# Optimization experiments

Measured on AMD Instinct MI355X. Metric: run time of the kernel, lower is better.

Reference implementation:

```python
import jax, jax.numpy as jnp
import numpy as np

B, T, D = 64, 8, 512          # batch, num_tokens (= num_heads), hidden_size (= head_dim)
S = 512                       # history seq_len
NKV = 4                       # num_key_value_heads
G = T // NKV                  # num_key_value_groups
EPS = 1e-6
SCALE = D ** -0.5
NEG_INF = float('-inf')


def rmsnorm(x, w):
    # Qwen3NextRMSNorm: norm in fp32, scale by (1 + weight), cast back
    xf = x.astype(jnp.float32)
    n = xf * jax.lax.rsqrt(jnp.mean(xf * xf, axis=-1, keepdims=True) + EPS)
    return (n * (1.0 + w.astype(jnp.float32))).astype(x.dtype)


def setup_inputs() -> dict:
    key = jax.random.key(0)
    ks = jax.random.split(key, 8)
    return {
        'target_emb': jax.random.normal(ks[0], (B, T, D), dtype=jnp.float32),
        'history_emb': jax.random.normal(ks[1], (B, S, D), dtype=jnp.float32),
        'key_padding_mask': jax.random.bernoulli(ks[2], 0.2, (B, S)),
        'q_proj_w': jax.random.normal(ks[3], (D, D), dtype=jnp.float32) * (D ** -0.5),
        'k_proj_w': jax.random.normal(ks[4], (NKV * D, D), dtype=jnp.float32) * (D ** -0.5),
        'v_proj_w': jax.random.normal(ks[5], (NKV * D, D), dtype=jnp.float32) * (D ** -0.5),
        'q_norm_w': jnp.zeros((D,), dtype=jnp.float32),
        'k_norm_w': jnp.zeros((D,), dtype=jnp.float32),
    }


def reference(target_emb, history_emb, key_padding_mask,
              q_proj_w, k_proj_w, v_proj_w, q_norm_w, k_norm_w):
    # q_proj on flattened tokens: [B,T,D] @ W^T -> [B,T,D]
    q = jnp.einsum('btd,ed->bte', target_emb, q_proj_w)
    q = rmsnorm(q, q_norm_w)
    # k/v projections: [B,S,D] -> [B,S,NKV,D]
    k = jnp.einsum('bsd,ed->bse', history_emb, k_proj_w).reshape(B, S, NKV, D)
    v = jnp.einsum('bsd,ed->bse', history_emb, v_proj_w).reshape(B, S, NKV, D)
    k = rmsnorm(k, k_norm_w)
    # group queries by kv head instead of materializing repeat_kv copies
    qg = q.reshape(B, NKV, G, D)              # [B,NKV,G,D]
    kt = jnp.transpose(k, (0, 2, 1, 3))        # [B,NKV,S,D]
    vt = jnp.transpose(v, (0, 2, 1, 3))        # [B,NKV,S,D]
    scores = jnp.einsum('bngd,bnsd->bngs', qg, kt) * SCALE  # [B,NKV,G,S]
    bias = jnp.where(key_padding_mask, NEG_INF, 0.0).astype(jnp.float32)
    scores = scores + bias[:, None, None, :]
    attn = jax.nn.softmax(scores.astype(jnp.float32), axis=-1).astype(q.dtype)
    out = jnp.einsum('bngs,bnsd->bngd', attn, vt)  # [B,NKV,G,D]
    tokens = out.reshape(B, T, D)
    attn_weights = attn.reshape(B, T, 1, S)       # matches torch [B,H,1,S]
    return (tokens, attn_weights)
```

## Files before the change

kernel.cpp:

```cpp
#include <hip/hip_runtime.h>
#include <stdint.h>

#define NB 64
#define NT 8
#define ND 512
#define NS 512
#define NKV 4
#define BSLICE 32
#define NSLICE (NB / BSLICE)

typedef __attribute__((ext_vector_type(8))) short short8_t;
typedef __attribute__((ext_vector_type(8))) unsigned short ushort8_t;
typedef __attribute__((ext_vector_type(4))) float f32x4;

typedef const __attribute__((address_space(1))) void gas_void;
typedef __attribute__((address_space(3))) void las_void;

#define HSP_HI 0ull
#define WKH_B  16777216ull
#define WVH_B  18874368ull
#define WKT_B  20971520ull
#define THI_B  23068672ull
#define TLO_B  23592960ull
#define QWH_B  24117248ull
#define QWL_B  24641536ull
#define QP_B   25165824ull
#define WFF_B  26214400ull
#define OUTF_B 27262976ull
#define SSQ_B  28311552ull
#define MASK_B 28835840ull
#define PBUF_B 28966912ull
#define DOT_B  30015488ull
#define QPH_B  31064064ull
#define QPL_B  31588352ull
#define WFH_B  32112640ull
#define WFL_B  32636928ull
#define HH_B   33161216ull
#define HL_B   33685504ull
#define FLAG_B 34209792ull
#define ZERO_CNT 917504

__device__ __forceinline__ float b2f(unsigned short u) {
    union { unsigned int i; float f; } x; x.i = ((unsigned int)u) << 16; return x.f;
}
__device__ __forceinline__ unsigned short f2b(float f) {
    union { float f; unsigned int i; } x; x.f = f;
    unsigned int i = x.i;
    unsigned int r = i + 0x7FFFu + ((i >> 16) & 1u);
    return (unsigned short)(r >> 16);
}
__device__ __forceinline__ float in_elem(const void* p, long long i, int is_f32) {
    return is_f32 ? ((const float*)p)[i] : b2f(((const unsigned short*)p)[i]);
}
__device__ __forceinline__ void store_out(void* out, int is_f32, size_t idx, float v) {
    if (is_f32) ((float*)out)[idx] = v;
    else        ((unsigned short*)out)[idx] = f2b(v);
}

__global__ __launch_bounds__(256) void scan_zero_kernel(const unsigned short* __restrict__ hraw,
                                                        const void* __restrict__ mraw,
                                                        int* __restrict__ flag,
                                                        float* __restrict__ zbase) {
    const int tid = threadIdx.x;
    const int bx = blockIdx.x;
    if (bx >= 2) {
        zbase[(size_t)(bx - 2) * 256 + tid] = 0.0f;
        return;
    }
    if (bx == 0) {
        __shared__ int cnt;
        if (tid == 0) cnt = 0;
        __syncthreads();
        int c = 0;
#pragma unroll
        for (int it = 0; it < 16; ++it) {
            unsigned int e = (hraw[tid + it * 256] >> 7) & 0xFFu;
            if (e >= 0xF0u) ++c;
        }
        if (c) atomicAdd(&cnt, c);
        __syncthreads();
        if (tid == 0) flag[0] = (cnt >= 8) ? 1 : 0;
    } else {
        __shared__ int s_bf16, s_f32, s_not01, s_oddnz;
        if (tid == 0) { s_bf16 = 0; s_f32 = 0; s_not01 = 0; s_oddnz = 0; }
        __syncthreads();
        const unsigned int* w32 = (const unsigned int*)mraw;
        int f_bf16 = 0, f_f32 = 0, f_not01 = 0, f_oddnz = 0;
#pragma unroll
        for (int it = 0; it < 32; ++it) {
            const int i = tid + it * 256;
            unsigned int w = w32[i];
            if (w == 0x00003F80u || w == 0x3F803F80u) f_bf16 = 1;
            if (w == 0x3F800000u) f_f32 = 1;
            if (w != 0u && w != 1u && w != 0x3F800000u) f_not01 = 1;
            if ((i & 1) && w != 0u) f_oddnz = 1;
        }
        if (f_bf16)  s_bf16 = 1;
        if (f_f32)   s_f32 = 1;
        if (f_not01) s_not01 = 1;
        if (f_oddnz) s_oddnz = 1;
        __syncthreads();
        if (tid == 0) {
            int mode;
            if (s_bf16)       mode = 3;
            else if (s_f32)   mode = 0;
            else if (s_not01) mode = 1;
            else if (s_oddnz) mode = 0;
            else              mode = 2;
            flag[1] = mode;
        }
    }
}

__device__ __forceinline__ void split8(const void* src, long long i8, int is_f32,
                                       ushort8_t& h, ushort8_t& l) {
    if (is_f32) {
        const float* s = (const float*)src + i8;
        float4 a = *(const float4*)s;
        float4 b = *(const float4*)(s + 4);
        float v[8] = {a.x, a.y, a.z, a.w, b.x, b.y, b.z, b.w};
#pragma unroll
        for (int j = 0; j < 8; ++j) {
            unsigned short hh = f2b(v[j]);
            h[j] = hh;
            l[j] = f2b(v[j] - b2f(hh));
        }
    } else {
        h = *(const ushort8_t*)((const unsigned short*)src + i8);
#pragma unroll
        for (int j = 0; j < 8; ++j) l[j] = 0;
    }
}
__device__ __forceinline__ ushort8_t hi8(const void* src, long long i8, int is_f32) {
    ushort8_t h;
    if (is_f32) {
        const float* s = (const float*)src + i8;
        float4 a = *(const float4*)s;
        float4 b = *(const float4*)(s + 4);
        float v[8] = {a.x, a.y, a.z, a.w, b.x, b.y, b.z, b.w};
#pragma unroll
        for (int j = 0; j < 8; ++j) h[j] = f2b(v[j]);
    } else {
        h = *(const ushort8_t*)((const unsigned short*)src + i8);
    }
    return h;
}

__global__ __launch_bounds__(256) void prep_kernel(const void* __restrict__ target,
                                                   const void* __restrict__ Wq,
                                                   const void* __restrict__ Wk,
                                                   const void* __restrict__ Wv,
                                                   unsigned short* __restrict__ tHi,
                                                   unsigned short* __restrict__ tLo,
                                                   unsigned short* __restrict__ qwHi,
                                                   unsigned short* __restrict__ qwLo,
                                                   unsigned short* __restrict__ wkHi,
                                                   unsigned short* __restrict__ wvHi,
                                                   unsigned short* __restrict__ wkT,
                                                   const int* __restrict__ flag) {
    __shared__ unsigned short tile[64][65];
    const int bx = blockIdx.x;
    const int tid = threadIdx.x;
    const int is_f32 = flag[0];
    if (bx < 128) {
        const long long i8 = ((long long)bx * 256 + tid) * 8;
        ushort8_t h, l;
        split8(target, i8, is_f32, h, l);
        *(ushort8_t*)(tHi + i8) = h;
        *(ushort8_t*)(tLo + i8) = l;
    } else if (bx < 256) {
        const long long i8 = ((long long)(bx - 128) * 256 + tid) * 8;
        ushort8_t h, l;
        split8(Wq, i8, is_f32, h, l);
        *(ushort8_t*)(qwHi + i8) = h;
        *(ushort8_t*)(qwLo + i8) = l;
    } else if (bx < 768) {
        const long long i8 = ((long long)(bx - 256) * 256 + tid) * 8;
        *(ushort8_t*)(wkHi + i8) = hi8(Wk, i8, is_f32);
    } else if (bx < 1280) {
        const long long i8 = ((long long)(bx - 768) * 256 + tid) * 8;
        *(ushort8_t*)(wvHi + i8) = hi8(Wv, i8, is_f32);
    } else {
        const int idx = bx - 1280;
        const int e0 = (idx & 31) * 64, d0 = (idx >> 5) * 64;
        const int tx = tid & 63, ty = tid >> 6;
#pragma unroll
        for (int i = 0; i < 16; ++i) {
            const int er = ty + 4 * i;
            tile[er][tx] = f2b(in_elem(Wk, (long long)(e0 + er) * 512 + d0 + tx, is_f32));
        }
        __syncthreads();
        const int n = e0 >> 9, eLoc = (e0 & 511);
#pragma unroll
        for (int i = 0; i < 16; ++i) {
            const int d = d0 + ty + 4 * i;
            wkT[(size_t)n * 512 * 512 + (size_t)d * 512 + eLoc + tx] = tile[tx][ty + 4 * i];
        }
    }
}

__global__ __launch_bounds__(256) void presplit_hist_kernel(const void* __restrict__ src,
                                                            unsigned short* __restrict__ hi,
                                                            const int* __restrict__ flag,
                                                            long long elemOff) {
    const long long i8 = ((long long)blockIdx.x * 256 + threadIdx.x) * 8;
    *(ushort8_t*)(hi + i8) = hi8(src, elemOff + i8, flag[0]);
}


__device__ __forceinline__ void mfma2_tile(const unsigned short* __restrict__ Ah,
                                           const unsigned short* __restrict__ Al,
                                           const unsigned short* __restrict__ B,
                                           unsigned short* AsH, unsigned short* AsL,
                                           unsigned short* Bs,
                                           int m0, int n0, int tid,
                                           int ktBeg, int ktEnd,
                                           f32x4 acc[4][4]) {
    const int lane = tid & 63, wave = tid >> 6;
    const int wr = wave >> 1, wc = wave & 1;
    const int lr = lane & 15, lq = lane >> 4;
#pragma unroll
    for (int i = 0; i < 4; ++i)
#pragma unroll
        for (int j = 0; j < 4; ++j) acc[i][j] = (f32x4){0.f, 0.f, 0.f, 0.f};

    for (int kt = ktBeg; kt < ktEnd; ++kt) {
        const int k0 = kt << 5;
#pragma unroll
        for (int i = 0; i < 2; ++i) {
            const int c = i * 256 + tid;
            const size_t aoff = (size_t)(m0 + (c >> 2)) * 512 + (k0 + (c & 3) * 8);
            const size_t boff = (size_t)(n0 + (c >> 2)) * 512 + (k0 + (c & 3) * 8);
            __builtin_amdgcn_global_load_lds((gas_void*)(Ah + aoff), (las_void*)(AsH + c * 8), 16, 0, 0);
            __builtin_amdgcn_global_load_lds((gas_void*)(Al + aoff), (las_void*)(AsL + c * 8), 16, 0, 0);
            __builtin_amdgcn_global_load_lds((gas_void*)(B + boff), (las_void*)(Bs + c * 8), 16, 0, 0);
        }
        __syncthreads();
        short8_t aH[4], aL[4], bF[4];
#pragma unroll
        for (int t = 0; t < 4; ++t) {
            const int ao = (wr * 64 + t * 16 + lr) * 32 + lq * 8;
            aH[t] = *(const short8_t*)(AsH + ao);
            aL[t] = *(const short8_t*)(AsL + ao);
            bF[t] = *(const short8_t*)(Bs + (wc * 64 + t * 16 + lr) * 32 + lq * 8);
        }
#pragma unroll
        for (int ti = 0; ti < 4; ++ti)
#pragma unroll
            for (int tj = 0; tj < 4; ++tj)
                acc[ti][tj] = __builtin_amdgcn_mfma_f32_16x16x32_bf16(aH[ti], bF[tj], acc[ti][tj], 0, 0, 0);
#pragma unroll
        for (int ti = 0; ti < 4; ++ti)
#pragma unroll
            for (int tj = 0; tj < 4; ++tj)
                acc[ti][tj] = __builtin_amdgcn_mfma_f32_16x16x32_bf16(aL[ti], bF[tj], acc[ti][tj], 0, 0, 0);
        __syncthreads();
    }
}

__device__ __forceinline__ void mfma3_tile(const unsigned short* __restrict__ Ah,
                                           const unsigned short* __restrict__ Al,
                                           const unsigned short* __restrict__ Bh,
                                           const unsigned short* __restrict__ Bl,
                                           unsigned short* AsH, unsigned short* AsL,
                                           unsigned short* BsH, unsigned short* BsL,
                                           int m0, int n0, int tid,
                                           int ktBeg, int ktEnd,
                                           f32x4 acc[4][4]) {
    const int lane = tid & 63, wave = tid >> 6;
    const int wr = wave >> 1, wc = wave & 1;
    const int lr = lane & 15, lq = lane >> 4;
#pragma unroll
    for (int i = 0; i < 4; ++i)
#pragma unroll
        for (int j = 0; j < 4; ++j) acc[i][j] = (f32x4){0.f, 0.f, 0.f, 0.f};

    for (int kt = ktBeg; kt < ktEnd; ++kt) {
        const int k0 = kt << 5;
#pragma unroll
        for (int i = 0; i < 2; ++i) {
            const int c = i * 256 + tid;
            const size_t aoff = (size_t)(m0 + (c >> 2)) * 512 + (k0 + (c & 3) * 8);
            const size_t boff = (size_t)(n0 + (c >> 2)) * 512 + (k0 + (c & 3) * 8);
            __builtin_amdgcn_global_load_lds((gas_void*)(Ah + aoff), (las_void*)(AsH + c * 8), 16, 0, 0);
            __builtin_amdgcn_global_load_lds((gas_void*)(Al + aoff), (las_void*)(AsL + c * 8), 16, 0, 0);
            __builtin_amdgcn_global_load_lds((gas_void*)(Bh + boff), (las_void*)(BsH + c * 8), 16, 0, 0);
            __builtin_amdgcn_global_load_lds((gas_void*)(Bl + boff), (las_void*)(BsL + c * 8), 16, 0, 0);
        }
        __syncthreads();
        short8_t aH[4], aL[4], bH[4], bL[4];
#pragma unroll
        for (int t = 0; t < 4; ++t) {
            const int ao = (wr * 64 + t * 16 + lr) * 32 + lq * 8;
            const int bo = (wc * 64 + t * 16 + lr) * 32 + lq * 8;
            aH[t] = *(const short8_t*)(AsH + ao);
            aL[t] = *(const short8_t*)(AsL + ao);
            bH[t] = *(const short8_t*)(BsH + bo);
            bL[t] = *(const short8_t*)(BsL + bo);
        }
#pragma unroll
        for (int ti = 0; ti < 4; ++ti)
#pragma unroll
            for (int tj = 0; tj < 4; ++tj)
                acc[ti][tj] = __builtin_amdgcn_mfma_f32_16x16x32_bf16(aH[ti], bH[tj], acc[ti][tj], 0, 0, 0);
#pragma unroll
        for (int ti = 0; ti < 4; ++ti)
#pragma unroll
            for (int tj = 0; tj < 4; ++tj)
                acc[ti][tj] = __builtin_amdgcn_mfma_f32_16x16x32_bf16(aH[ti], bL[tj], acc[ti][tj], 0, 0, 0);
#pragma unroll
        for (int ti = 0; ti < 4; ++ti)
#pragma unroll
            for (int tj = 0; tj < 4; ++tj)
                acc[ti][tj] = __builtin_amdgcn_mfma_f32_16x16x32_bf16(aL[ti], bH[tj], acc[ti][tj], 0, 0, 0);
        __syncthreads();
    }
}

__global__ __launch_bounds__(256) void gemm3_ks(const unsigned short* __restrict__ Ah,
                                                const unsigned short* __restrict__ Al,
                                                const unsigned short* __restrict__ Bh,
                                                const unsigned short* __restrict__ Bl,
                                                float* __restrict__ C) {
    __shared__ __align__(16) unsigned short AsH[128 * 32];
    __shared__ __align__(16) unsigned short AsL[128 * 32];
    __shared__ __align__(16) unsigned short BsH[128 * 32];
    __shared__ __align__(16) unsigned short BsL[128 * 32];
    const int m0 = blockIdx.x * 128, n0 = blockIdx.y * 128;
    const int kt0 = blockIdx.z * 4;
    const int tid = threadIdx.x;
    f32x4 acc[4][4];
    mfma3_tile(Ah, Al, Bh, Bl, AsH, AsL, BsH, BsL, m0, n0, tid, kt0, kt0 + 4, acc);
    const int lane = tid & 63, wave = tid >> 6;
    const int wr = wave >> 1, wc = wave & 1;
    const int lr = lane & 15, lq = lane >> 4;
#pragma unroll
    for (int ti = 0; ti < 4; ++ti)
#pragma unroll
        for (int tj = 0; tj < 4; ++tj)
#pragma unroll
            for (int r = 0; r < 4; ++r) {
                const int row = m0 + wr * 64 + ti * 16 + lq * 4 + r;
                const int col = n0 + wc * 64 + tj * 16 + lr;
                atomicAdd(&C[(size_t)row * 512 + col], acc[ti][tj][r]);
            }
}

__global__ __launch_bounds__(64) void rmsnorm_qperm(const float* __restrict__ q,
                                                    const void* __restrict__ qnw,
                                                    const void* __restrict__ knw,
                                                    unsigned short* __restrict__ qpHi,
                                                    unsigned short* __restrict__ qpLo,
                                                    const int* __restrict__ flag) {
    const int row = blockIdx.x;
    const int lane = threadIdx.x;
    const int is_f32 = flag[0];
    const float* p = q + (size_t)row * ND + lane * 8;
    float v[8];
    float4 a = *(const float4*)p;
    float4 b4 = *(const float4*)(p + 4);
    v[0] = a.x; v[1] = a.y; v[2] = a.z; v[3] = a.w;
    v[4] = b4.x; v[5] = b4.y; v[6] = b4.z; v[7] = b4.w;
    float ssq = 0.f;
#pragma unroll
    for (int j = 0; j < 8; ++j) ssq = fmaf(v[j], v[j], ssq);
#pragma unroll
    for (int off = 1; off < 64; off <<= 1) ssq += __shfl_xor(ssq, off);
    float r = rsqrtf(ssq * (1.0f / ND) + 1e-6f);
    const float SCALE = 0.044194173824159216f;
    const int b = row >> 3, h = row & 7;
    const int prow = (h >> 1) * 128 + b * 2 + (h & 1);
    ushort8_t hh, ll;
#pragma unroll
    for (int j = 0; j < 8; ++j) {
        int e = lane * 8 + j;
        float val = v[j] * r * (1.0f + in_elem(qnw, e, is_f32)) * (1.0f + in_elem(knw, e, is_f32)) * SCALE;
        unsigned short hv = f2b(val);
        hh[j] = hv; ll[j] = f2b(val - b2f(hv));
    }
    *(ushort8_t*)(qpHi + (size_t)prow * 512 + lane * 8) = hh;
    *(ushort8_t*)(qpLo + (size_t)prow * 512 + lane * 8) = ll;
}

__global__ __launch_bounds__(256) void wfold_ks(const unsigned short* __restrict__ qpHi,
                                                const unsigned short* __restrict__ qpLo,
                                                const unsigned short* __restrict__ wkT,
                                                float* __restrict__ wfF) {
    __shared__ __align__(16) unsigned short AsH[128 * 32];
    __shared__ __align__(16) unsigned short AsL[128 * 32];
    __shared__ __align__(16) unsigned short Bs[128 * 32];
    const int n = blockIdx.x;
    const int m0 = n * 128, n0 = blockIdx.y * 128;
    const int kt0 = blockIdx.z * 4;
    const int tid = threadIdx.x;
    f32x4 acc[4][4];
    mfma2_tile(qpHi, qpLo, wkT + (size_t)n * 512 * 512, AsH, AsL, Bs, m0, n0, tid, kt0, kt0 + 4, acc);

    const int lane = tid & 63, wave = tid >> 6;
    const int wr = wave >> 1, wc = wave & 1;
    const int lr = lane & 15, lq = lane >> 4;
#pragma unroll
    for (int ti = 0; ti < 4; ++ti)
#pragma unroll
        for (int tj = 0; tj < 4; ++tj)
#pragma unroll
            for (int r = 0; r < 4; ++r) {
                const int row = m0 + wr * 64 + ti * 16 + lq * 4 + r;
                const int d = n0 + wc * 64 + tj * 16 + lr;
                atomicAdd(&wfF[(size_t)row * 512 + d], acc[ti][tj][r]);
            }
}

#define SSQ8_ABUF(b) ((b) * 32768)
#define SSQ8_BBUF(b) (65536 + (b) * 32768)

#define SSQ8_STAGE_A(r, tt, bufOff)                                                       \
    do {                                                                                  \
        const int rcA0_ = rl0 + (r) * 64;                                                 \
        __builtin_amdgcn_global_load_lds(                                                 \
            (gas_void*)(A + (size_t)(mBase + rcA0_) * 512 + (tt) * 64 + ksw),             \
            (las_void*)(smem + (bufOff) + rcA0_ * 128 + k0 * 2), 16, 0, 0);               \
        const int rcA1_ = rcA0_ + 128;                                                    \
        __builtin_amdgcn_global_load_lds(                                                 \
            (gas_void*)(A + (size_t)(mBase + rcA1_) * 512 + (tt) * 64 + ksw),             \
            (las_void*)(smem + (bufOff) + rcA1_ * 128 + k0 * 2), 16, 0, 0);               \
    } while (0)

#define SSQ8_STAGE_B(q, tt, bufOff)                                                       \
    do {                                                                                  \
        const int rcB0_ = bR + (q) * 32;                                                  \
        __builtin_amdgcn_global_load_lds(                                                 \
            (gas_void*)(W + (size_t)(nBase + rcB0_) * 512 + (tt) * 64 + ksw),             \
            (las_void*)(smem + (bufOff) + rcB0_ * 128 + k0 * 2), 16, 0, 0);               \
        const int rcB1_ = rcB0_ + 128;                                                    \
        __builtin_amdgcn_global_load_lds(                                                 \
            (gas_void*)(W + (size_t)(nBase + rcB1_) * 512 + (tt) * 64 + ksw),             \
            (las_void*)(smem + (bufOff) + rcB1_ * 128 + k0 * 2), 16, 0, 0);               \
    } while (0)

#define SSQ8_READ_A(qm, bufOff)                                                           \
    _Pragma("unroll")                                                                     \
    for (int m_ = 0; m_ < 4; ++m_) {                                                      \
        const int rc_ = wm * 128 + (qm) * 64 + m_ * 16 + lr;                              \
        af[m_][0] = *(const short8_t*)(smem + (bufOff) + rc_ * 128 + kb0);                \
        af[m_][1] = *(const short8_t*)(smem + (bufOff) + rc_ * 128 + kb1);                \
    }

#define SSQ8_READ_B2(nh, bufOff)                                                          \
    _Pragma("unroll")                                                                     \
    for (int n_ = 0; n_ < 2; ++n_) {                                                      \
        const int cc_ = wn * 64 + (nh) * 32 + n_ * 16 + lr;                               \
        bf[(nh) * 2 + n_][0] = *(const short8_t*)(smem + (bufOff) + cc_ * 128 + kb0);     \
        bf[(nh) * 2 + n_][1] = *(const short8_t*)(smem + (bufOff) + cc_ * 128 + kb1);     \
    }

#define SSQ8_MFMA_Q(qm, nh)                                                               \
    _Pragma("unroll")                                                                     \
    for (int m_ = 0; m_ < 4; ++m_)                                                        \
    _Pragma("unroll")                                                                     \
    for (int n_ = 0; n_ < 2; ++n_) {                                                      \
        acc[(qm) * 4 + m_][(nh) * 2 + n_] = __builtin_amdgcn_mfma_f32_16x16x32_bf16(      \
            af[m_][0], bf[(nh) * 2 + n_][0], acc[(qm) * 4 + m_][(nh) * 2 + n_], 0, 0, 0); \
        acc[(qm) * 4 + m_][(nh) * 2 + n_] = __builtin_amdgcn_mfma_f32_16x16x32_bf16(      \
            af[m_][1], bf[(nh) * 2 + n_][1], acc[(qm) * 4 + m_][(nh) * 2 + n_], 0, 0, 0); \
    }

#define SSQ8_SYNC_PRE()                                                                   \
    __builtin_amdgcn_s_barrier();                                                         \
    asm volatile("s_waitcnt lgkmcnt(0)" ::: "memory");                                    \
    __builtin_amdgcn_sched_barrier(0);                                                    \
    __builtin_amdgcn_s_setprio(1);

#define SSQ8_SYNC_POST()                                                                  \
    __builtin_amdgcn_s_setprio(0);                                                        \
    __builtin_amdgcn_s_barrier();

__global__ __launch_bounds__(512) void gemm_ssq8(const unsigned short* __restrict__ A,
                                                 const unsigned short* __restrict__ W,
                                                 float* __restrict__ ssq, int b0) {
    extern __shared__ char smem[];
    const int tid = threadIdx.x;
    const int lane = tid & 63, wave = tid >> 6;
    const int wm = wave >> 2, wn = wave & 3;
    const int lr = lane & 15, lq = lane >> 4;
    const int mBase = blockIdx.x * 256;
    const int nBase = blockIdx.y * 256;

    const int rl0 = tid >> 3;
    const int k0 = (tid & 7) << 3;
    const int ksw = k0 ^ ((rl0 & 7) << 3);
    const int bR = (rl0 & 31) | ((rl0 >> 5) << 6);

    const int kb0 = ((lq * 8) ^ ((lr & 7) << 3)) * 2;
    const int kb1 = ((32 + lq * 8) ^ ((lr & 7) << 3)) * 2;

    f32x4 acc[8][4];
#pragma unroll
    for (int i = 0; i < 8; ++i)
#pragma unroll
        for (int j = 0; j < 4; ++j) acc[i][j] = (f32x4){0.f, 0.f, 0.f, 0.f};

    SSQ8_STAGE_A(0, 0, SSQ8_ABUF(0));
    SSQ8_STAGE_B(0, 0, SSQ8_BBUF(0));
    SSQ8_STAGE_A(1, 0, SSQ8_ABUF(0));
    SSQ8_STAGE_B(1, 0, SSQ8_BBUF(0));
    SSQ8_STAGE_A(0, 1, SSQ8_ABUF(1));
    SSQ8_STAGE_B(0, 1, SSQ8_BBUF(1));
    asm volatile("s_waitcnt vmcnt(4)" ::: "memory");
    __builtin_amdgcn_s_barrier();

    short8_t af[4][2], bf[4][2];

#pragma unroll
    for (int t = 0; t < 8; ++t) {
        const int cur = t & 1, nxt = cur ^ 1;
        const int aC = SSQ8_ABUF(cur), bC = SSQ8_BBUF(cur);
        const int aN = SSQ8_ABUF(nxt), bN = SSQ8_BBUF(nxt);
        SSQ8_READ_A(0, aC)
        SSQ8_READ_B2(0, bC)
        if (t + 1 < 8) SSQ8_STAGE_A(1, t + 1, aN);
        SSQ8_SYNC_PRE()
        SSQ8_MFMA_Q(0, 0)
        SSQ8_SYNC_POST()
        SSQ8_READ_B2(1, bC)
        if (t + 1 < 8) SSQ8_STAGE_B(1, t + 1, bN);
        SSQ8_SYNC_PRE()
        SSQ8_MFMA_Q(0, 1)
        SSQ8_SYNC_POST()
        SSQ8_READ_A(1, aC)
        if (t + 2 < 8) SSQ8_STAGE_A(0, t + 2, aC);
        SSQ8_SYNC_PRE()
        SSQ8_MFMA_Q(1, 0)
        SSQ8_SYNC_POST()
        if (t + 2 < 8) SSQ8_STAGE_B(0, t + 2, bC);
        __builtin_amdgcn_s_barrier();
        __builtin_amdgcn_sched_barrier(0);
        __builtin_amdgcn_s_setprio(1);
        SSQ8_MFMA_Q(1, 1)
        __builtin_amdgcn_s_setprio(0);
        if (t < 6) {
            asm volatile("s_waitcnt vmcnt(4)" ::: "memory");
        } else if (t == 6) {
            asm volatile("s_waitcnt vmcnt(0)" ::: "memory");
        }
        __builtin_amdgcn_s_barrier();
    }

    const int nIdx = (int)(blockIdx.y >> 1);
#pragma unroll
    for (int m = 0; m < 8; ++m)
#pragma unroll
        for (int r = 0; r < 4; ++r) {
            float v = 0.f;
#pragma unroll
            for (int n = 0; n < 4; ++n) {
                float x = acc[m][n][r];
                v = fmaf(x, x, v);
            }
#pragma unroll
            for (int off = 1; off < 16; off <<= 1) v += __shfl_xor(v, off);
            if (lr == 0) {
                const int srow = mBase + wm * 128 + m * 16 + lq * 4 + r;
                const int bn = (b0 + (srow >> 9)) * 4 + nIdx;
                atomicAdd(&ssq[(size_t)bn * 512 + (srow & 511)], v);
            }
        }
}

__global__ __launch_bounds__(256) void dot_slice_kernel(const unsigned short* __restrict__ hspHi,
                                                        const float* __restrict__ wfF,
                                                        float* __restrict__ dot,
                                                        int b0) {
    const int bl = blockIdx.x;
    const int bG = b0 + bl;
    const int tid = threadIdx.x;
    const int wave = tid >> 6, lane = tid & 63;
    const int lr = lane & 15, lq = lane >> 4;
    const int sW = blockIdx.y * 64 + wave * 16;

    const int h = lr;
    const int valid = (h < 8);
    const size_t wrow = (size_t)((h >> 1) * 128 + bG * 2 + (h & 1)) * 512;
    const size_t arow = ((size_t)bl * 512 + sW + lr) * 512;
    const float4 zf4 = {0.f, 0.f, 0.f, 0.f};

    f32x4 acc = {0.f, 0.f, 0.f, 0.f};
    for (int kt = 0; kt < 16; ++kt) {
        const int ko = kt * 32 + lq * 8;
        short8_t aF = *(const short8_t*)(hspHi + arow + ko);
        float4 wa = valid ? *(const float4*)(wfF + wrow + ko) : zf4;
        float4 wb = valid ? *(const float4*)(wfF + wrow + ko + 4) : zf4;
        float wv[8] = {wa.x, wa.y, wa.z, wa.w, wb.x, wb.y, wb.z, wb.w};
        short8_t bH, bL;
#pragma unroll
        for (int j = 0; j < 8; ++j) {
            unsigned short hv = f2b(wv[j]);
            bH[j] = (short)hv;
            bL[j] = (short)f2b(wv[j] - b2f(hv));
        }
        acc = __builtin_amdgcn_mfma_f32_16x16x32_bf16(aF, bH, acc, 0, 0, 0);
        acc = __builtin_amdgcn_mfma_f32_16x16x32_bf16(aF, bL, acc, 0, 0, 0);
    }
    if (valid) {
        const int n = h >> 1, g = h & 1;
        const size_t base = ((size_t)(bG * 4 + n) * 2 + g) * 512;
#pragma unroll
        for (int r = 0; r < 4; ++r) {
            const int s = sW + lq * 4 + r;
            dot[base + s] = acc[r];
        }
    }
}

__global__ __launch_bounds__(512) void softmax_slice(const float* __restrict__ ssq,
                                                     const float* __restrict__ dot,
                                                     const void* __restrict__ mraw,
                                                     float* __restrict__ pbuf,
                                                     void* __restrict__ out,
                                                     const int* __restrict__ flag,
                                                     int b0) {
    const int bn = b0 * 4 + blockIdx.x;
    const int b = bn >> 2;
    const int tid = threadIdx.x;
    const int wave = tid >> 6, lane = tid & 63;
    const int is_f32 = flag[0];
    const int mode = flag[1];
    __shared__ float red[32];

    float sq = ssq[(size_t)bn * 512 + tid];
    float rms = rsqrtf(sq * (1.0f / ND) + 1e-6f);
    const int mi = b * NS + tid;
    int masked;
    if (mode == 3)      masked = (((const unsigned short*)mraw)[mi] != 0);
    else if (mode == 1) masked = (((const unsigned char*)mraw)[mi] != 0);
    else if (mode == 0) masked = (((const unsigned int*)mraw)[mi] != 0u);
    else                masked = (((const unsigned int*)mraw)[2 * mi] != 0u);
    float ninf = -__builtin_inff();
    float v0 = masked ? ninf : dot[((size_t)bn * 2 + 0) * 512 + tid] * rms;
    float v1 = masked ? ninf : dot[((size_t)bn * 2 + 1) * 512 + tid] * rms;

    float m0 = v0, m1 = v1;
#pragma unroll
    for (int off = 1; off < 64; off <<= 1) {
        m0 = fmaxf(m0, __shfl_xor(m0, off));
        m1 = fmaxf(m1, __shfl_xor(m1, off));
    }
    if (lane == 0) { red[wave] = m0; red[8 + wave] = m1; }
    __syncthreads();
    m0 = red[0]; m1 = red[8];
#pragma unroll
    for (int w = 1; w < 8; ++w) { m0 = fmaxf(m0, red[w]); m1 = fmaxf(m1, red[8 + w]); }
    float e0 = __expf(v0 - m0), e1 = __expf(v1 - m1);
    float su0 = e0, su1 = e1;
#pragma unroll
    for (int off = 1; off < 64; off <<= 1) {
        su0 += __shfl_xor(su0, off);
        su1 += __shfl_xor(su1, off);
    }
    if (lane == 0) { red[16 + wave] = su0; red[24 + wave] = su1; }
    __syncthreads();
    float t0 = 0.f, t1 = 0.f;
#pragma unroll
    for (int w = 0; w < 8; ++w) { t0 += red[16 + w]; t1 += red[24 + w]; }
    float p0 = e0 / t0, p1 = e1 / t1;

    pbuf[((size_t)bn * 2 + 0) * 512 + tid] = p0;
    pbuf[((size_t)bn * 2 + 1) * 512 + tid] = p1;
    size_t abase = 262144u + (size_t)bn * 1024 + tid;
    store_out(out, is_f32, abase, p0);
    store_out(out, is_f32, abase + 512, p1);
}

__global__ __launch_bounds__(512) void htilde_kernel(const unsigned short* __restrict__ hspHi,
                                                     const float* __restrict__ pbuf,
                                                     unsigned short* __restrict__ hHi,
                                                     unsigned short* __restrict__ hLo,
                                                     int b0) {
    __shared__ float pl[8][512];
    __shared__ float red[8][64][8];
    const int bl = blockIdx.x;
    const int bG = b0 + bl;
    const int d0 = blockIdx.y * 64;
    const int tid = threadIdx.x;
#pragma unroll
    for (int k = 0; k < 8; ++k) {
        const int j = tid + k * 512;
        const int h = j >> 9, s = j & 511;
        pl[h][s] = pbuf[((size_t)(bG * 4 + (h >> 1)) * 2 + (h & 1)) * 512 + s];
    }
    __syncthreads();

    const int dl = tid & 63, sl = tid >> 6;
    const unsigned short* hb = hspHi + (size_t)bl * 512 * 512 + d0 + dl;
    float acc[8];
#pragma unroll
    for (int h = 0; h < 8; ++h) acc[h] = 0.f;
#pragma unroll 4
    for (int i = 0; i < 64; ++i) {
        const int s = i * 8 + sl;
        float hv = b2f(hb[(size_t)s * 512]);
#pragma unroll
        for (int h = 0; h < 8; ++h) acc[h] = fmaf(pl[h][s], hv, acc[h]);
    }
#pragma unroll
    for (int h = 0; h < 8; ++h) red[sl][dl][h] = acc[h];
    __syncthreads();

    const int dl2 = tid >> 3, h2 = tid & 7;
    float v = 0.f;
#pragma unroll
    for (int s2 = 0; s2 < 8; ++s2) v += red[s2][dl2][h2];
    const int row = (h2 >> 1) * 128 + bG * 2 + (h2 & 1);
    unsigned short hv = f2b(v);
    hHi[(size_t)row * 512 + d0 + dl2] = hv;
    hLo[(size_t)row * 512 + d0 + dl2] = f2b(v - b2f(hv));
}

__global__ __launch_bounds__(256) void gemm_out_ks(const unsigned short* __restrict__ hHi,
                                                   const unsigned short* __restrict__ hLo,
                                                   const unsigned short* __restrict__ wvHi,
                                                   float* __restrict__ outF) {
    __shared__ __align__(16) unsigned short AsH[128 * 32];
    __shared__ __align__(16) unsigned short AsL[128 * 32];
    __shared__ __align__(16) unsigned short Bs[128 * 32];
    const int n = blockIdx.x;
    const int m0 = n * 128, n0 = blockIdx.y * 128;
    const int kt0 = blockIdx.z * 4;
    const int tid = threadIdx.x;
    f32x4 acc[4][4];
    mfma2_tile(hHi, hLo, wvHi + (size_t)n * 512 * 512, AsH, AsL, Bs, m0, n0, tid, kt0, kt0 + 4, acc);

    const int lane = tid & 63, wave = tid >> 6;
    const int wr = wave >> 1, wc = wave & 1;
    const int lr = lane & 15, lq = lane >> 4;
#pragma unroll
    for (int ti = 0; ti < 4; ++ti)
#pragma unroll
        for (int tj = 0; tj < 4; ++tj)
#pragma unroll
            for (int r = 0; r < 4; ++r) {
                const int row = m0 + wr * 64 + ti * 16 + lq * 4 + r;
                const int e = n0 + wc * 64 + tj * 16 + lr;
                atomicAdd(&outF[(size_t)row * 512 + e], acc[ti][tj][r]);
            }
}

__global__ __launch_bounds__(256) void out_final_kernel(const float* __restrict__ outF,
                                                        void* __restrict__ out,
                                                        const int* __restrict__ flag) {
    const size_t i = (size_t)blockIdx.x * 256 + threadIdx.x;
    const int row = (int)(i >> 9), e = (int)(i & 511);
    const int n = row >> 7, rl = row & 127;
    const int b = rl >> 1, g = rl & 1;
    store_out(out, flag[0], (size_t)(b * 8 + n * 2 + g) * 512 + e, outF[i]);
}

extern "C" void kernel_launch(void* const* d_in, const int* in_sizes, int n_in,
                              void* d_out, int out_size, void* d_ws, size_t ws_size,
                              hipStream_t stream) {
    (void)in_sizes; (void)n_in; (void)out_size; (void)ws_size;
    const void* target = d_in[0];
    const void* hist   = d_in[1];
    const void* mraw   = d_in[2];
    const void* Wq     = d_in[3];
    const void* Wk     = d_in[4];
    const void* Wv     = d_in[5];
    const void* qnw    = d_in[6];
    const void* knw    = d_in[7];

    char* w = (char*)d_ws;
    unsigned short* hspHi = (unsigned short*)(w + HSP_HI);
    unsigned short* wkHi  = (unsigned short*)(w + WKH_B);
    unsigned short* wvHi  = (unsigned short*)(w + WVH_B);
    unsigned short* wkT   = (unsigned short*)(w + WKT_B);
    unsigned short* tHi   = (unsigned short*)(w + THI_B);
    unsigned short* tLo   = (unsigned short*)(w + TLO_B);
    unsigned short* qwHi  = (unsigned short*)(w + QWH_B);
    unsigned short* qwLo  = (unsigned short*)(w + QWL_B);
    float* qp    = (float*)(w + QP_B);
    float* wfF   = (float*)(w + WFF_B);
    float* outF  = (float*)(w + OUTF_B);
    float* ssq   = (float*)(w + SSQ_B);
    float* pbuf  = (float*)(w + PBUF_B);
    float* dotb  = (float*)(w + DOT_B);
    unsigned short* qpHi = (unsigned short*)(w + QPH_B);
    unsigned short* qpLo = (unsigned short*)(w + QPL_B);
    unsigned short* hHi  = (unsigned short*)(w + HH_B);
    unsigned short* hLo  = (unsigned short*)(w + HL_B);
    int* flag = (int*)(w + FLAG_B);

    static bool attr_set = false;
    if (!attr_set) {
        (void)hipFuncSetAttribute(reinterpret_cast<const void*>(&gemm_ssq8),
                                  hipFuncAttributeMaxDynamicSharedMemorySize, 131072);
        attr_set = true;
    }

    scan_zero_kernel<<<2 + ZERO_CNT / 256, 256, 0, stream>>>(
        (const unsigned short*)hist, mraw, flag, qp);
    prep_kernel<<<1536, 256, 0, stream>>>(target, Wq, Wk, Wv, tHi, tLo, qwHi, qwLo,
                                          wkHi, wvHi, wkT, flag);

    gemm3_ks<<<dim3(4, 4, 4), 256, 0, stream>>>(tHi, tLo, qwHi, qwLo, qp);
    rmsnorm_qperm<<<NB * NT, 64, 0, stream>>>(qp, qnw, knw, qpHi, qpLo, flag);
    wfold_ks<<<dim3(4, 4, 4), 256, 0, stream>>>(qpHi, qpLo, wkT, wfF);

    for (int sl = 0; sl < NSLICE; ++sl) {
        const int b0 = sl * BSLICE;
        presplit_hist_kernel<<<4096, 256, 0, stream>>>(hist, hspHi, flag,
                                                       (long long)sl * BSLICE * 512 * 512);
        gemm_ssq8<<<dim3(64, 8), 512, 131072, stream>>>(hspHi, wkHi, ssq, b0);
        dot_slice_kernel<<<dim3(BSLICE, 8), 256, 0, stream>>>(hspHi, wfF, dotb, b0);
        softmax_slice<<<BSLICE * NKV, 512, 0, stream>>>(ssq, dotb, mraw, pbuf, d_out, flag, b0);
        htilde_kernel<<<dim3(BSLICE, 8), 512, 0, stream>>>(hspHi, pbuf, hHi, hLo, b0);
    }
    gemm_out_ks<<<dim3(4, 4, 4), 256, 0, stream>>>(hHi, hLo, wvHi, outF);
    out_final_kernel<<<1024, 256, 0, stream>>>(outF, d_out, flag);
}
```

Measured before the change: 288.1 us.

## Fuse q·k dot into K-projection epilogue, dropping weight folding and dot kernel

The query·key scores are now computed directly in the gemm_ssq8 epilogue by dotting the fp32 K-projection accumulators with the normalized, scaled query. They are accumulated with atomics next to the sum-of-squares. This removes the Wk transpose in prep, the wfold_ks GEMM that folded q into Wk, and the per-slice dot_slice_kernel that reread the history tensor. The costs are extra FMAs, shuffles and two more atomics per row in the GEMM epilogue. The scores also now rely on dotb lying inside the zeroed workspace region.

```diff
diff --git a/kernel.cpp b/kernel.cpp
--- a/kernel.cpp
+++ b/kernel.cpp
@@ -25,16 +25,11 @@
 #define QWH_B  24117248ull
 #define QWL_B  24641536ull
 #define QP_B   25165824ull
-#define WFF_B  26214400ull
+#define DOT_B  26214400ull
 #define OUTF_B 27262976ull
 #define SSQ_B  28311552ull
-#define MASK_B 28835840ull
 #define PBUF_B 28966912ull
-#define DOT_B  30015488ull
-#define QPH_B  31064064ull
-#define QPL_B  31588352ull
-#define WFH_B  32112640ull
-#define WFL_B  32636928ull
+#define QPF_B  31064064ull
 #define HH_B   33161216ull
 #define HL_B   33685504ull
 #define FLAG_B 34209792ull
@@ -156,9 +151,7 @@
                                                    unsigned short* __restrict__ qwLo,
                                                    unsigned short* __restrict__ wkHi,
                                                    unsigned short* __restrict__ wvHi,
-                                                   unsigned short* __restrict__ wkT,
                                                    const int* __restrict__ flag) {
-    __shared__ unsigned short tile[64][65];
     const int bx = blockIdx.x;
     const int tid = threadIdx.x;
     const int is_f32 = flag[0];
@@ -177,25 +170,9 @@
     } else if (bx < 768) {
         const long long i8 = ((long long)(bx - 256) * 256 + tid) * 8;
         *(ushort8_t*)(wkHi + i8) = hi8(Wk, i8, is_f32);
-    } else if (bx < 1280) {
+    } else {
         const long long i8 = ((long long)(bx - 768) * 256 + tid) * 8;
         *(ushort8_t*)(wvHi + i8) = hi8(Wv, i8, is_f32);
-    } else {
-        const int idx = bx - 1280;
-        const int e0 = (idx & 31) * 64, d0 = (idx >> 5) * 64;
-        const int tx = tid & 63, ty = tid >> 6;
-#pragma unroll
-        for (int i = 0; i < 16; ++i) {
-            const int er = ty + 4 * i;
-            tile[er][tx] = f2b(in_elem(Wk, (long long)(e0 + er) * 512 + d0 + tx, is_f32));
-        }
-        __syncthreads();
-        const int n = e0 >> 9, eLoc = (e0 & 511);
-#pragma unroll
-        for (int i = 0; i < 16; ++i) {
-            const int d = d0 + ty + 4 * i;
-            wkT[(size_t)n * 512 * 512 + (size_t)d * 512 + eLoc + tx] = tile[tx][ty + 4 * i];
-        }
     }
 }
 
@@ -349,8 +326,7 @@
 __global__ __launch_bounds__(64) void rmsnorm_qperm(const float* __restrict__ q,
                                                     const void* __restrict__ qnw,
                                                     const void* __restrict__ knw,
-                                                    unsigned short* __restrict__ qpHi,
-                                                    unsigned short* __restrict__ qpLo,
+                                                    float* __restrict__ qpF,
                                                     const int* __restrict__ flag) {
     const int row = blockIdx.x;
     const int lane = threadIdx.x;
@@ -370,45 +346,15 @@
     const float SCALE = 0.044194173824159216f;
     const int b = row >> 3, h = row & 7;
     const int prow = (h >> 1) * 128 + b * 2 + (h & 1);
-    ushort8_t hh, ll;
+    float o[8];
 #pragma unroll
     for (int j = 0; j < 8; ++j) {
         int e = lane * 8 + j;
-        float val = v[j] * r * (1.0f + in_elem(qnw, e, is_f32)) * (1.0f + in_elem(knw, e, is_f32)) * SCALE;
-        unsigned short hv = f2b(val);
-        hh[j] = hv; ll[j] = f2b(val - b2f(hv));
-    }
-    *(ushort8_t*)(qpHi + (size_t)prow * 512 + lane * 8) = hh;
-    *(ushort8_t*)(qpLo + (size_t)prow * 512 + lane * 8) = ll;
-}
-
-__global__ __launch_bounds__(256) void wfold_ks(const unsigned short* __restrict__ qpHi,
-                                                const unsigned short* __restrict__ qpLo,
-                                                const unsigned short* __restrict__ wkT,
-                                                float* __restrict__ wfF) {
-    __shared__ __align__(16) unsigned short AsH[128 * 32];
-    __shared__ __align__(16) unsigned short AsL[128 * 32];
-    __shared__ __align__(16) unsigned short Bs[128 * 32];
-    const int n = blockIdx.x;
-    const int m0 = n * 128, n0 = blockIdx.y * 128;
-    const int kt0 = blockIdx.z * 4;
-    const int tid = threadIdx.x;
-    f32x4 acc[4][4];
-    mfma2_tile(qpHi, qpLo, wkT + (size_t)n * 512 * 512, AsH, AsL, Bs, m0, n0, tid, kt0, kt0 + 4, acc);
-
-    const int lane = tid & 63, wave = tid >> 6;
-    const int wr = wave >> 1, wc = wave & 1;
-    const int lr = lane & 15, lq = lane >> 4;
-#pragma unroll
-    for (int ti = 0; ti < 4; ++ti)
-#pragma unroll
-        for (int tj = 0; tj < 4; ++tj)
-#pragma unroll
-            for (int r = 0; r < 4; ++r) {
-                const int row = m0 + wr * 64 + ti * 16 + lq * 4 + r;
-                const int d = n0 + wc * 64 + tj * 16 + lr;
-                atomicAdd(&wfF[(size_t)row * 512 + d], acc[ti][tj][r]);
-            }
+        o[j] = v[j] * r * (1.0f + in_elem(qnw, e, is_f32)) * (1.0f + in_elem(knw, e, is_f32)) * SCALE;
+    }
+    float4* dst = (float4*)(qpF + (size_t)prow * 512 + lane * 8);
+    dst[0] = (float4){o[0], o[1], o[2], o[3]};
+    dst[1] = (float4){o[4], o[5], o[6], o[7]};
 }
 
 #define SSQ8_ABUF(b) ((b) * 32768)
@@ -477,7 +423,10 @@
 
 __global__ __launch_bounds__(512) void gemm_ssq8(const unsigned short* __restrict__ A,
                                                  const unsigned short* __restrict__ W,
-                                                 float* __restrict__ ssq, int b0) {
+                                                 const float* __restrict__ qpF,
+                                                 float* __restrict__ ssq,
+                                                 float* __restrict__ dotb,
+                                                 int b0) {
     extern __shared__ char smem[];
     const int tid = threadIdx.x;
     const int lane = tid & 63, wave = tid >> 6;
@@ -546,70 +495,43 @@
         __builtin_amdgcn_s_barrier();
     }
 
-    const int nIdx = (int)(blockIdx.y >> 1);
+    const int nh = (int)(blockIdx.y >> 1);
+    const int bG = b0 + (mBase >> 9);
+    const int bn = bG * 4 + nh;
+    const int dBase = (nBase & 511) + wn * 64 + lr;
+    const size_t qrow0 = (size_t)(nh * 128 + bG * 2) * 512;
+    float qv0[4], qv1[4];
+#pragma unroll
+    for (int n = 0; n < 4; ++n) {
+        qv0[n] = qpF[qrow0 + dBase + n * 16];
+        qv1[n] = qpF[qrow0 + 512 + dBase + n * 16];
+    }
 #pragma unroll
     for (int m = 0; m < 8; ++m)
 #pragma unroll
         for (int r = 0; r < 4; ++r) {
-            float v = 0.f;
+            float v = 0.f, d0 = 0.f, d1 = 0.f;
 #pragma unroll
             for (int n = 0; n < 4; ++n) {
                 float x = acc[m][n][r];
                 v = fmaf(x, x, v);
+                d0 = fmaf(x, qv0[n], d0);
+                d1 = fmaf(x, qv1[n], d1);
             }
 #pragma unroll
-            for (int off = 1; off < 16; off <<= 1) v += __shfl_xor(v, off);
+            for (int off = 1; off < 16; off <<= 1) {
+                v += __shfl_xor(v, off);
+                d0 += __shfl_xor(d0, off);
+                d1 += __shfl_xor(d1, off);
+            }
             if (lr == 0) {
                 const int srow = mBase + wm * 128 + m * 16 + lq * 4 + r;
-                const int bn = (b0 + (srow >> 9)) * 4 + nIdx;
-                atomicAdd(&ssq[(size_t)bn * 512 + (srow & 511)], v);
+                const int s = srow & 511;
+                atomicAdd(&ssq[(size_t)bn * 512 + s], v);
+                atomicAdd(&dotb[((size_t)bn * 2 + 0) * 512 + s], d0);
+                atomicAdd(&dotb[((size_t)bn * 2 + 1) * 512 + s], d1);
             }
         }
-}
-
-__global__ __launch_bounds__(256) void dot_slice_kernel(const unsigned short* __restrict__ hspHi,
-                                                        const float* __restrict__ wfF,
-                                                        float* __restrict__ dot,
-                                                        int b0) {
-    const int bl = blockIdx.x;
-    const int bG = b0 + bl;
-    const int tid = threadIdx.x;
-    const int wave = tid >> 6, lane = tid & 63;
-    const int lr = lane & 15, lq = lane >> 4;
-    const int sW = blockIdx.y * 64 + wave * 16;
-
-    const int h = lr;
-    const int valid = (h < 8);
-    const size_t wrow = (size_t)((h >> 1) * 128 + bG * 2 + (h & 1)) * 512;
-    const size_t arow = ((size_t)bl * 512 + sW + lr) * 512;
-    const float4 zf4 = {0.f, 0.f, 0.f, 0.f};
-
-    f32x4 acc = {0.f, 0.f, 0.f, 0.f};
-    for (int kt = 0; kt < 16; ++kt) {
-        const int ko = kt * 32 + lq * 8;
-        short8_t aF = *(const short8_t*)(hspHi + arow + ko);
-        float4 wa = valid ? *(const float4*)(wfF + wrow + ko) : zf4;
-        float4 wb = valid ? *(const float4*)(wfF + wrow + ko + 4) : zf4;
-        float wv[8] = {wa.x, wa.y, wa.z, wa.w, wb.x, wb.y, wb.z, wb.w};
-        short8_t bH, bL;
-#pragma unroll
-        for (int j = 0; j < 8; ++j) {
-            unsigned short hv = f2b(wv[j]);
-            bH[j] = (short)hv;
-            bL[j] = (short)f2b(wv[j] - b2f(hv));
-        }
-        acc = __builtin_amdgcn_mfma_f32_16x16x32_bf16(aF, bH, acc, 0, 0, 0);
-        acc = __builtin_amdgcn_mfma_f32_16x16x32_bf16(aF, bL, acc, 0, 0, 0);
-    }
-    if (valid) {
-        const int n = h >> 1, g = h & 1;
-        const size_t base = ((size_t)(bG * 4 + n) * 2 + g) * 512;
-#pragma unroll
-        for (int r = 0; r < 4; ++r) {
-            const int s = sW + lq * 4 + r;
-            dot[base + s] = acc[r];
-        }
-    }
 }
 
 __global__ __launch_bounds__(512) void softmax_slice(const float* __restrict__ ssq,
@@ -772,19 +694,16 @@
     unsigned short* hspHi = (unsigned short*)(w + HSP_HI);
     unsigned short* wkHi  = (unsigned short*)(w + WKH_B);
     unsigned short* wvHi  = (unsigned short*)(w + WVH_B);
-    unsigned short* wkT   = (unsigned short*)(w + WKT_B);
     unsigned short* tHi   = (unsigned short*)(w + THI_B);
     unsigned short* tLo   = (unsigned short*)(w + TLO_B);
     unsigned short* qwHi  = (unsigned short*)(w + QWH_B);
     unsigned short* qwLo  = (unsigned short*)(w + QWL_B);
     float* qp    = (float*)(w + QP_B);
-    float* wfF   = (float*)(w + WFF_B);
+    float* dotb  = (float*)(w + DOT_B);
     float* outF  = (float*)(w + OUTF_B);
     float* ssq   = (float*)(w + SSQ_B);
     float* pbuf  = (float*)(w + PBUF_B);
-    float* dotb  = (float*)(w + DOT_B);
-    unsigned short* qpHi = (unsigned short*)(w + QPH_B);
-    unsigned short* qpLo = (unsigned short*)(w + QPL_B);
+    float* qpF   = (float*)(w + QPF_B);
     unsigned short* hHi  = (unsigned short*)(w + HH_B);
     unsigned short* hLo  = (unsigned short*)(w + HL_B);
     int* flag = (int*)(w + FLAG_B);
@@ -798,19 +717,17 @@
 
     scan_zero_kernel<<<2 + ZERO_CNT / 256, 256, 0, stream>>>(
         (const unsigned short*)hist, mraw, flag, qp);
-    prep_kernel<<<1536, 256, 0, stream>>>(target, Wq, Wk, Wv, tHi, tLo, qwHi, qwLo,
-                                          wkHi, wvHi, wkT, flag);
+    prep_kernel<<<1280, 256, 0, stream>>>(target, Wq, Wk, Wv, tHi, tLo, qwHi, qwLo,
+                                          wkHi, wvHi, flag);
 
     gemm3_ks<<<dim3(4, 4, 4), 256, 0, stream>>>(tHi, tLo, qwHi, qwLo, qp);
-    rmsnorm_qperm<<<NB * NT, 64, 0, stream>>>(qp, qnw, knw, qpHi, qpLo, flag);
-    wfold_ks<<<dim3(4, 4, 4), 256, 0, stream>>>(qpHi, qpLo, wkT, wfF);
+    rmsnorm_qperm<<<NB * NT, 64, 0, stream>>>(qp, qnw, knw, qpF, flag);
 
     for (int sl = 0; sl < NSLICE; ++sl) {
         const int b0 = sl * BSLICE;
         presplit_hist_kernel<<<4096, 256, 0, stream>>>(hist, hspHi, flag,
                                                        (long long)sl * BSLICE * 512 * 512);
-        gemm_ssq8<<<dim3(64, 8), 512, 131072, stream>>>(hspHi, wkHi, ssq, b0);
-        dot_slice_kernel<<<dim3(BSLICE, 8), 256, 0, stream>>>(hspHi, wfF, dotb, b0);
+        gemm_ssq8<<<dim3(64, 8), 512, 131072, stream>>>(hspHi, wkHi, qpF, ssq, dotb, b0);
         softmax_slice<<<BSLICE * NKV, 512, 0, stream>>>(ssq, dotb, mraw, pbuf, d_out, flag, b0);
         htilde_kernel<<<dim3(BSLICE, 8), 512, 0, stream>>>(hspHi, pbuf, hHi, hLo, b0);
     }
```

Result: slower. 308.6 us (+7.1%).
